# Performance work log

Hardware: AMD Instinct MI355X
Metric: run time of the kernel (lower is better)

The kernel has to match this reference:

```python
import jax, jax.numpy as jnp
import numpy as np

N = 50000       # nodes
E = 800000      # edges (avg degree 16)
D_IN = 96
D_OUT = 96
K = 3           # Chebyshev order
EPS = 1e-5      # BatchNorm eps


def setup_inputs() -> dict:
    key = jax.random.key(0)
    k1, k2, k3 = jax.random.split(key, 3)
    x = jax.random.normal(k1, (N, D_IN), dtype=jnp.float32)
    edge_index = jax.random.randint(k2, (2, E), 0, N)
    # ChebConv weights: one [D_IN, D_OUT] matrix per Chebyshev order + shared bias
    W = jax.random.normal(k3, (K, D_IN, D_OUT), dtype=jnp.float32) * (1.0 / np.sqrt(D_IN))
    bias = jnp.zeros((D_OUT,), dtype=jnp.float32)
    # BatchNorm1d affine params
    gamma = jnp.ones((D_OUT,), dtype=jnp.float32)
    beta = jnp.zeros((D_OUT,), dtype=jnp.float32)
    return {"x": x, "edge_index": edge_index, "W": W, "bias": bias,
            "gamma": gamma, "beta": beta}


def _cheb_edge_norm(edge_index, num_nodes):
    # PyG ChebConv.__norm__ with normalization='sym', lambda_max=2.0:
    # L_hat = 2L/lambda_max - I = -D^{-1/2} A D^{-1/2} (self loops removed, diag 0)
    row, col = edge_index[0], edge_index[1]
    w = jnp.where(row != col, 1.0, 0.0)  # remove self loops (weight 0 == removed)
    deg = jax.ops.segment_sum(w, row, num_segments=num_nodes)
    dis = jnp.where(deg > 0, jax.lax.rsqrt(jnp.maximum(deg, 1e-12)), 0.0)
    return -dis[row] * w * dis[col]  # [E]


def reference(x, edge_index, W, bias, gamma, beta):
    row, col = edge_index[0], edge_index[1]
    norm = _cheb_edge_norm(edge_index, N)

    def prop(h):  # sparse L_hat @ h via gather + scatter-add
        return jax.ops.segment_sum(norm[:, None] * h[row], col, num_segments=N)

    # Chebyshev recursion: T0 = x, T1 = L_hat x, Tk = 2 L_hat T_{k-1} - T_{k-2}
    Tx0 = x
    out = Tx0 @ W[0]
    Tx1 = prop(Tx0)
    out = out + Tx1 @ W[1]
    for k in range(2, K):
        Tx2 = 2.0 * prop(Tx1) - Tx0
        out = out + Tx2 @ W[k]
        Tx0, Tx1 = Tx1, Tx2
    out = out + bias

    # BatchNorm1d (training mode: batch stats over nodes, biased variance)
    mean = out.mean(axis=0)
    var = out.var(axis=0)
    return (out - mean) * jax.lax.rsqrt(var + EPS) * gamma + beta
```

## Files before the change

### kernel.cpp

```cpp
#include <hip/hip_runtime.h>

#define N_NODES 50000
#define N_EDGES 800000
#define D 96
#define DH 48
#define CAP 48
#define HG 64
#define W4 (N_NODES / 4)
#define EPS_BN 1e-5f

typedef short bf16x8 __attribute__((ext_vector_type(8)));
typedef float f32x4  __attribute__((ext_vector_type(4)));
union frag_cvt { uint4 u; bf16x8 f; };

__device__ __forceinline__ unsigned pack_bf16(float a, float b) {
    unsigned ua = __float_as_uint(a), ub = __float_as_uint(b);
    ua = (ua + 0x7fffu + ((ua >> 16) & 1u)) >> 16;
    ub = (ub + 0x7fffu + ((ub >> 16) & 1u)) >> 16;
    return (ua & 0xffffu) | (ub << 16);
}
__device__ __forceinline__ unsigned bf16_hi_bits(float a) {
    unsigned u = __float_as_uint(a);
    return (u + 0x7fffu + ((u >> 16) & 1u)) & 0xffff0000u;
}
__device__ __forceinline__ float bf16_lo(unsigned u) { return __uint_as_float(u << 16); }
__device__ __forceinline__ float bf16_hi(unsigned u) { return __uint_as_float(u & 0xffff0000u); }

#define CB ((N_NODES * DH + 1023) / 1024)
__global__ __launch_bounds__(1024) void prep_hist_kernel(
        const int* __restrict__ ei, unsigned* __restrict__ rowpart,
        unsigned* __restrict__ colpart, const float* __restrict__ x,
        unsigned* __restrict__ xh, const float* __restrict__ W,
        unsigned* __restrict__ wswz) {
    if (blockIdx.x < HG) {
        __shared__ unsigned h[W4];
        const int chunk = N_EDGES / HG;
        const int e0 = blockIdx.x * chunk;
        int rs[13], cs[13];
        int n = 0;
        for (int e = e0 + threadIdx.x; e < e0 + chunk; e += 1024, ++n) {
            rs[n] = ei[e];
            cs[n] = ei[N_EDGES + e];
        }
        for (int w = threadIdx.x; w < W4; w += 1024) h[w] = 0;
        __syncthreads();
        for (int i = 0; i < n; ++i)
            if (rs[i] != cs[i]) atomicAdd(&h[rs[i] >> 2], 1u << ((rs[i] & 3) * 8));
        __syncthreads();
        unsigned* rp = rowpart + (size_t)blockIdx.x * W4;
        for (int w = threadIdx.x; w < W4; w += 1024) rp[w] = h[w];
        __syncthreads();
        for (int w = threadIdx.x; w < W4; w += 1024) h[w] = 0;
        __syncthreads();
        for (int i = 0; i < n; ++i)
            if (rs[i] != cs[i]) atomicAdd(&h[cs[i] >> 2], 1u << ((cs[i] & 3) * 8));
        __syncthreads();
        unsigned* cp = colpart + (size_t)blockIdx.x * W4;
        for (int w = threadIdx.x; w < W4; w += 1024) cp[w] = h[w];
    } else if (blockIdx.x < HG + CB) {
        int t = (blockIdx.x - HG) * 1024 + threadIdx.x;
        if (t >= N_NODES * DH) return;
        float2 v = ((const float2*)x)[t];
        xh[t] = pack_bf16(v.x, v.y);
    } else {
        int t = (blockIdx.x - HG - CB) * 1024 + threadIdx.x;
        if (t >= 3 * 3 * 6 * 64) return;
        int lane = t & 63;
        int rest = t >> 6;
        int tile = rest % 6; rest /= 6;
        int q    = rest % 3;
        int s    = rest / 3;
        int n     = tile * 16 + (lane & 15);
        int kbase = q * 32 + (lane >> 4) * 8;
        uint4 u;
        const float* Wk = W + ((size_t)s * D + kbase) * D + n;
        u.x = pack_bf16(Wk[0 * D], Wk[1 * D]);
        u.y = pack_bf16(Wk[2 * D], Wk[3 * D]);
        u.z = pack_bf16(Wk[4 * D], Wk[5 * D]);
        u.w = pack_bf16(Wk[6 * D], Wk[7 * D]);
        ((uint4*)wswz)[t] = u;
    }
}

__global__ void reduce_kernel(unsigned* __restrict__ colpart,
                              const unsigned* __restrict__ rowpart,
                              int* __restrict__ cnt, float* __restrict__ dis,
                              float* __restrict__ stats) {
    if (blockIdx.x == 0 && threadIdx.x < 2 * D) stats[threadIdx.x] = 0.f;
    int w = blockIdx.x * blockDim.x + threadIdx.x;
    if (w >= W4) return;
    unsigned run = 0;
    for (int b = 0; b < HG; ++b) {
        unsigned v = colpart[(size_t)b * W4 + w];
        colpart[(size_t)b * W4 + w] = run;
        run += v;
    }
    int4 c4;
    c4.x = run & 0xffu; c4.y = (run >> 8) & 0xffu;
    c4.z = (run >> 16) & 0xffu; c4.w = run >> 24;
    ((int4*)cnt)[w] = c4;
    unsigned s0 = 0, s1 = 0, s2 = 0, s3 = 0;
    for (int b = 0; b < HG; ++b) {
        unsigned v = rowpart[(size_t)b * W4 + w];
        s0 += v & 0xffu; s1 += (v >> 8) & 0xffu;
        s2 += (v >> 16) & 0xffu; s3 += v >> 24;
    }
    float4 o;
    o.x = s0 ? rsqrtf((float)s0) : 0.f;
    o.y = s1 ? rsqrtf((float)s1) : 0.f;
    o.z = s2 ? rsqrtf((float)s2) : 0.f;
    o.w = s3 ? rsqrtf((float)s3) : 0.f;
    ((float4*)dis)[w] = o;
}

__global__ __launch_bounds__(1024) void place_kernel(const int* __restrict__ ei,
                                                     const unsigned* __restrict__ colpart,
                                                     const float* __restrict__ dis,
                                                     unsigned* __restrict__ ent) {
    __shared__ unsigned h[W4];
    const unsigned* pref = colpart + (size_t)blockIdx.x * W4;
    for (int w = threadIdx.x; w < W4; w += 1024) h[w] = pref[w];
    __syncthreads();
    const int chunk = N_EDGES / HG;
    const int e0 = blockIdx.x * chunk;
    for (int e = e0 + threadIdx.x; e < e0 + chunk; e += 1024) {
        int r = ei[e];
        int c = ei[N_EDGES + e];
        if (r == c) continue;
        float w = -dis[r] * dis[c];
        int sh = (c & 3) * 8;
        unsigned old = atomicAdd(&h[c >> 2], 1u << sh);
        int pos = (old >> sh) & 0xff;
        if (pos < CAP) ent[c * CAP + pos] = bf16_hi_bits(w) | (unsigned)r;
    }
}

template <int MODE>
__global__ __launch_bounds__(256) void prop_gather_kernel(
        const int* __restrict__ cnt_arr, const unsigned* __restrict__ ent,
        const unsigned* __restrict__ hp, const float* __restrict__ x,
        unsigned* __restrict__ out_h) {
    int nodeA = blockIdx.x * 8 + (threadIdx.x >> 6) * 2;
    int nodeB = nodeA + 1;
    int lane = threadIdx.x & 63;
    if (nodeA >= N_NODES) return;
    const int cl = (lane < DH) ? lane : (lane - DH);
    int cntA = cnt_arr[nodeA]; if (cntA > CAP) cntA = CAP;
    int cntB = cnt_arr[nodeB]; if (cntB > CAP) cntB = CAP;
    unsigned elA = (lane < cntA) ? ent[nodeA * CAP + lane] : 0u;
    unsigned elB = (lane < cntB) ? ent[nodeB * CAP + lane] : 0u;
    float a0 = 0.f, a1 = 0.f, b0 = 0.f, b1 = 0.f;
    int cmax = cntA > cntB ? cntA : cntB;
    for (int j = 0; j < cmax; j += 24) {
        unsigned eeA[24], eeB[24];
        #pragma unroll
        for (int i = 0; i < 24; ++i) {
            eeA[i] = (unsigned)__shfl((int)elA, j + i, 64);
            eeB[i] = (unsigned)__shfl((int)elB, j + i, 64);
        }
        unsigned uuA[24], uuB[24];
        #pragma unroll
        for (int i = 0; i < 24; ++i)
            uuA[i] = hp[(eeA[i] & 0xffffu) * DH + cl];
        #pragma unroll
        for (int i = 0; i < 24; ++i)
            uuB[i] = hp[(eeB[i] & 0xffffu) * DH + cl];
        #pragma unroll
        for (int i = 0; i < 24; ++i) {
            float wA = __uint_as_float(eeA[i] & 0xffff0000u);
            a0 = fmaf(wA, bf16_lo(uuA[i]), a0);
            a1 = fmaf(wA, bf16_hi(uuA[i]), a1);
            float wB = __uint_as_float(eeB[i] & 0xffff0000u);
            b0 = fmaf(wB, bf16_lo(uuB[i]), b0);
            b1 = fmaf(wB, bf16_hi(uuB[i]), b1);
        }
    }
    if (lane < DH) {
        if (MODE == 0) {
            out_h[nodeA * DH + cl] = pack_bf16(a0, a1);
            out_h[nodeB * DH + cl] = pack_bf16(b0, b1);
        } else {
            float2 xA = ((const float2*)x)[nodeA * DH + cl];
            float2 xB = ((const float2*)x)[nodeB * DH + cl];
            out_h[nodeA * DH + cl] = pack_bf16(fmaf(2.f, a0, -xA.x),
                                               fmaf(2.f, a1, -xA.y));
            out_h[nodeB * DH + cl] = pack_bf16(fmaf(2.f, b0, -xB.x),
                                               fmaf(2.f, b1, -xB.y));
        }
    }
}

__global__ __launch_bounds__(256) void mfma_gemm_kernel(
        const unsigned* __restrict__ xh, const unsigned* __restrict__ t1h,
        const unsigned* __restrict__ t2h, const unsigned* __restrict__ wswz,
        float* __restrict__ out, float* __restrict__ stats) {
    const int wave = threadIdx.x >> 6;
    const int lane = threadIdx.x & 63;
    const int m    = lane & 15;
    const int kg   = lane >> 4;
    const int nb   = blockIdx.x * 128 + wave * 32;
    __shared__ float ssum[4][D], ssq[4][D];

    int arow0 = nb + m;       if (arow0 > N_NODES - 1) arow0 = N_NODES - 1;
    int arow1 = nb + 16 + m;  if (arow1 > N_NODES - 1) arow1 = N_NODES - 1;

    const unsigned* bases[3] = {xh, t1h, t2h};

    f32x4 acc[2][6];
    #pragma unroll
    for (int h = 0; h < 2; ++h)
        #pragma unroll
        for (int t = 0; t < 6; ++t) acc[h][t] = (f32x4){0.f, 0.f, 0.f, 0.f};

    #pragma unroll
    for (int s = 0; s < 3; ++s) {
        const unsigned* A0 = bases[s] + (size_t)arow0 * DH + kg * 4;
        const unsigned* A1 = bases[s] + (size_t)arow1 * DH + kg * 4;
        #pragma unroll
        for (int q = 0; q < 3; ++q) {
            frag_cvt a0, a1;
            a0.u = *(const uint4*)(A0 + q * 16);
            a1.u = *(const uint4*)(A1 + q * 16);
            const uint4* Bp = (const uint4*)wswz + (size_t)((s * 3 + q) * 6) * 64 + lane;
            #pragma unroll
            for (int t = 0; t < 6; ++t) {
                frag_cvt b;
                b.u = Bp[t * 64];
                acc[0][t] = __builtin_amdgcn_mfma_f32_16x16x32_bf16(a0.f, b.f, acc[0][t], 0, 0, 0);
                acc[1][t] = __builtin_amdgcn_mfma_f32_16x16x32_bf16(a1.f, b.f, acc[1][t], 0, 0, 0);
            }
        }
    }

    #pragma unroll
    for (int t = 0; t < 6; ++t) {
        int col = t * 16 + m;
        float s1 = 0.f, s2 = 0.f;
        #pragma unroll
        for (int h = 0; h < 2; ++h) {
            #pragma unroll
            for (int r = 0; r < 4; ++r) {
                int g = nb + h * 16 + kg * 4 + r;
                if (g < N_NODES) {
                    float o = acc[h][t][r];
                    out[(size_t)g * D + col] = o;
                    s1 += o;
                    s2 += o * o;
                }
            }
        }
        s1 += __shfl_xor(s1, 16, 64); s2 += __shfl_xor(s2, 16, 64);
        s1 += __shfl_xor(s1, 32, 64); s2 += __shfl_xor(s2, 32, 64);
        if (lane < 16) { ssum[wave][col] = s1; ssq[wave][col] = s2; }
    }
    __syncthreads();
    if (threadIdx.x < D) {
        int c = threadIdx.x;
        float s1 = ssum[0][c] + ssum[1][c] + ssum[2][c] + ssum[3][c];
        float s2 = ssq [0][c] + ssq [1][c] + ssq [2][c] + ssq [3][c];
        atomicAdd(&stats[c],     s1);
        atomicAdd(&stats[D + c], s2);
    }
}

__global__ void bn_kernel(float* __restrict__ o, const float* __restrict__ stats,
                          const float* __restrict__ gamma, const float* __restrict__ beta) {
    __shared__ __align__(16) float s_sc[D], s_sh[D];
    if (threadIdx.x < D) {
        int c = threadIdx.x;
        const float invN = 1.f / (float)N_NODES;
        float mean = stats[c] * invN;
        float var  = stats[D + c] * invN - mean * mean;
        float inv  = rsqrtf(fmaxf(var, 0.f) + EPS_BN);
        float sc   = gamma[c] * inv;
        s_sc[c] = sc;
        s_sh[c] = beta[c] - mean * sc;
    }
    __syncthreads();
    int t = blockIdx.x * blockDim.x + threadIdx.x;
    if (t >= N_NODES * (D / 4)) return;
    int c4 = t % (D / 4);
    float4 v  = ((float4*)o)[t];
    float4 sc = *(const float4*)(s_sc + c4 * 4);
    float4 sh = *(const float4*)(s_sh + c4 * 4);
    v.x = fmaf(v.x, sc.x, sh.x);
    v.y = fmaf(v.y, sc.y, sh.y);
    v.z = fmaf(v.z, sc.z, sh.z);
    v.w = fmaf(v.w, sc.w, sh.w);
    ((float4*)o)[t] = v;
}

extern "C" void kernel_launch(void* const* d_in, const int* in_sizes, int n_in,
                              void* d_out, int out_size, void* d_ws, size_t ws_size,
                              hipStream_t stream) {
    const float* x     = (const float*)d_in[0];
    const int*   ei    = (const int*)  d_in[1];
    const float* W     = (const float*)d_in[2];
    const float* bias  = (const float*)d_in[3];
    const float* gamma = (const float*)d_in[4];
    const float* beta  = (const float*)d_in[5];
    float* out = (float*)d_out;
    (void)bias;

    float*    stats   = (float*)d_ws;
    float*    dis     = stats + 2 * D;
    int*      cnt     = (int*)(dis + N_NODES);
    unsigned* ent     = (unsigned*)(cnt + N_NODES);
    unsigned* xh      = ent + (size_t)N_NODES * CAP;
    unsigned* t1h     = xh  + (size_t)N_NODES * DH;
    unsigned* t2h     = t1h + (size_t)N_NODES * DH;
    unsigned* wswz    = t2h + (size_t)N_NODES * DH;
    unsigned* rowpart = t2h;
    unsigned* colpart = t2h + (size_t)HG * W4;

    prep_hist_kernel<<<HG + CB + 4, 1024, 0, stream>>>(ei, rowpart, colpart,
                                                       x, xh, W, wswz);
    reduce_kernel<<<(W4 + 255) / 256, 256, 0, stream>>>(colpart, rowpart, cnt,
                                                        dis, stats);
    place_kernel<<<HG, 1024, 0, stream>>>(ei, colpart, dis, ent);

    const int prop_blocks = N_NODES / 8;
    prop_gather_kernel<0><<<prop_blocks, 256, 0, stream>>>(cnt, ent, xh,  nullptr, t1h);
    prop_gather_kernel<1><<<prop_blocks, 256, 0, stream>>>(cnt, ent, t1h, x,       t2h);

    mfma_gemm_kernel<<<(N_NODES + 127) / 128, 256, 0, stream>>>(
        xh, t1h, t2h, wswz, out, stats);

    bn_kernel<<<(N_NODES * (D / 4) + 255) / 256, 256, 0, stream>>>(out, stats, gamma, beta);
}
```

Measured before the change: 214.9 us.

## Replace LDS partitioned histogram CSR build with global atomics

Replaces the three-kernel graph preprocessing (per-block LDS byte-packed histograms, prefix reduction, LDS-based placement) with a memset, one prep kernel doing global atomic degree counts alongside the casts, and a placement kernel using global atomicAdd on per-column slot counters. This removes the serial 64-way prefix loop and the partial-histogram traffic, and saves a launch. The cost is contended global atomics over 800k edges instead of cheap LDS atomics. Edge order within each node's bucket also becomes nondeterministic, which changes the floating-point summation order.

```diff
diff --git a/kernel.cpp b/kernel.cpp
--- a/kernel.cpp
+++ b/kernel.cpp
@@ -5,8 +5,6 @@
 #define D 96
 #define DH 48
 #define CAP 48
-#define HG 64
-#define W4 (N_NODES / 4)
 #define EPS_BN 1e-5f
 
 typedef short bf16x8 __attribute__((ext_vector_type(8)));
@@ -26,44 +24,23 @@
 __device__ __forceinline__ float bf16_lo(unsigned u) { return __uint_as_float(u << 16); }
 __device__ __forceinline__ float bf16_hi(unsigned u) { return __uint_as_float(u & 0xffff0000u); }
 
-#define CB ((N_NODES * DH + 1023) / 1024)
-__global__ __launch_bounds__(1024) void prep_hist_kernel(
-        const int* __restrict__ ei, unsigned* __restrict__ rowpart,
-        unsigned* __restrict__ colpart, const float* __restrict__ x,
-        unsigned* __restrict__ xh, const float* __restrict__ W,
-        unsigned* __restrict__ wswz) {
-    if (blockIdx.x < HG) {
-        __shared__ unsigned h[W4];
-        const int chunk = N_EDGES / HG;
-        const int e0 = blockIdx.x * chunk;
-        int rs[13], cs[13];
-        int n = 0;
-        for (int e = e0 + threadIdx.x; e < e0 + chunk; e += 1024, ++n) {
-            rs[n] = ei[e];
-            cs[n] = ei[N_EDGES + e];
-        }
-        for (int w = threadIdx.x; w < W4; w += 1024) h[w] = 0;
-        __syncthreads();
-        for (int i = 0; i < n; ++i)
-            if (rs[i] != cs[i]) atomicAdd(&h[rs[i] >> 2], 1u << ((rs[i] & 3) * 8));
-        __syncthreads();
-        unsigned* rp = rowpart + (size_t)blockIdx.x * W4;
-        for (int w = threadIdx.x; w < W4; w += 1024) rp[w] = h[w];
-        __syncthreads();
-        for (int w = threadIdx.x; w < W4; w += 1024) h[w] = 0;
-        __syncthreads();
-        for (int i = 0; i < n; ++i)
-            if (rs[i] != cs[i]) atomicAdd(&h[cs[i] >> 2], 1u << ((cs[i] & 3) * 8));
-        __syncthreads();
-        unsigned* cp = colpart + (size_t)blockIdx.x * W4;
-        for (int w = threadIdx.x; w < W4; w += 1024) cp[w] = h[w];
-    } else if (blockIdx.x < HG + CB) {
-        int t = (blockIdx.x - HG) * 1024 + threadIdx.x;
-        if (t >= N_NODES * DH) return;
+#define CAST_BLK (N_NODES * DH / 256)
+#define EDGE_BLK (N_EDGES / 256)
+__global__ __launch_bounds__(256) void prep2_kernel(
+        const int* __restrict__ ei, int* __restrict__ deg,
+        const float* __restrict__ x, unsigned* __restrict__ xh,
+        const float* __restrict__ W, unsigned* __restrict__ wswz) {
+    if (blockIdx.x < CAST_BLK) {
+        int t = blockIdx.x * 256 + threadIdx.x;
         float2 v = ((const float2*)x)[t];
         xh[t] = pack_bf16(v.x, v.y);
+    } else if (blockIdx.x < CAST_BLK + EDGE_BLK) {
+        int e = (blockIdx.x - CAST_BLK) * 256 + threadIdx.x;
+        int r = ei[e];
+        int c = ei[N_EDGES + e];
+        if (r != c) atomicAdd(&deg[r], 1);
     } else {
-        int t = (blockIdx.x - HG - CB) * 1024 + threadIdx.x;
+        int t = (blockIdx.x - CAST_BLK - EDGE_BLK) * 256 + threadIdx.x;
         if (t >= 3 * 3 * 6 * 64) return;
         int lane = t & 63;
         int rest = t >> 6;
@@ -82,57 +59,18 @@
     }
 }
 
-__global__ void reduce_kernel(unsigned* __restrict__ colpart,
-                              const unsigned* __restrict__ rowpart,
-                              int* __restrict__ cnt, float* __restrict__ dis,
-                              float* __restrict__ stats) {
-    if (blockIdx.x == 0 && threadIdx.x < 2 * D) stats[threadIdx.x] = 0.f;
-    int w = blockIdx.x * blockDim.x + threadIdx.x;
-    if (w >= W4) return;
-    unsigned run = 0;
-    for (int b = 0; b < HG; ++b) {
-        unsigned v = colpart[(size_t)b * W4 + w];
-        colpart[(size_t)b * W4 + w] = run;
-        run += v;
-    }
-    int4 c4;
-    c4.x = run & 0xffu; c4.y = (run >> 8) & 0xffu;
-    c4.z = (run >> 16) & 0xffu; c4.w = run >> 24;
-    ((int4*)cnt)[w] = c4;
-    unsigned s0 = 0, s1 = 0, s2 = 0, s3 = 0;
-    for (int b = 0; b < HG; ++b) {
-        unsigned v = rowpart[(size_t)b * W4 + w];
-        s0 += v & 0xffu; s1 += (v >> 8) & 0xffu;
-        s2 += (v >> 16) & 0xffu; s3 += v >> 24;
-    }
-    float4 o;
-    o.x = s0 ? rsqrtf((float)s0) : 0.f;
-    o.y = s1 ? rsqrtf((float)s1) : 0.f;
-    o.z = s2 ? rsqrtf((float)s2) : 0.f;
-    o.w = s3 ? rsqrtf((float)s3) : 0.f;
-    ((float4*)dis)[w] = o;
-}
-
-__global__ __launch_bounds__(1024) void place_kernel(const int* __restrict__ ei,
-                                                     const unsigned* __restrict__ colpart,
-                                                     const float* __restrict__ dis,
-                                                     unsigned* __restrict__ ent) {
-    __shared__ unsigned h[W4];
-    const unsigned* pref = colpart + (size_t)blockIdx.x * W4;
-    for (int w = threadIdx.x; w < W4; w += 1024) h[w] = pref[w];
-    __syncthreads();
-    const int chunk = N_EDGES / HG;
-    const int e0 = blockIdx.x * chunk;
-    for (int e = e0 + threadIdx.x; e < e0 + chunk; e += 1024) {
-        int r = ei[e];
-        int c = ei[N_EDGES + e];
-        if (r == c) continue;
-        float w = -dis[r] * dis[c];
-        int sh = (c & 3) * 8;
-        unsigned old = atomicAdd(&h[c >> 2], 1u << sh);
-        int pos = (old >> sh) & 0xff;
-        if (pos < CAP) ent[c * CAP + pos] = bf16_hi_bits(w) | (unsigned)r;
-    }
+__global__ __launch_bounds__(256) void place2_kernel(
+        const int* __restrict__ ei, const int* __restrict__ deg,
+        int* __restrict__ pos, unsigned* __restrict__ ent) {
+    int e = blockIdx.x * 256 + threadIdx.x;
+    int r = ei[e];
+    int c = ei[N_EDGES + e];
+    if (r == c) return;
+    int dr = deg[r];
+    int dc = deg[c];
+    float w = (dc > 0) ? -rsqrtf((float)dr) * rsqrtf((float)dc) : 0.f;
+    int p = atomicAdd(&pos[c], 1);
+    if (p < CAP) ent[c * CAP + p] = bf16_hi_bits(w) | (unsigned)r;
 }
 
 template <int MODE>
@@ -302,26 +240,25 @@
     float* out = (float*)d_out;
     (void)bias;
 
-    float*    stats   = (float*)d_ws;
-    float*    dis     = stats + 2 * D;
-    int*      cnt     = (int*)(dis + N_NODES);
-    unsigned* ent     = (unsigned*)(cnt + N_NODES);
-    unsigned* xh      = ent + (size_t)N_NODES * CAP;
-    unsigned* t1h     = xh  + (size_t)N_NODES * DH;
-    unsigned* t2h     = t1h + (size_t)N_NODES * DH;
-    unsigned* wswz    = t2h + (size_t)N_NODES * DH;
-    unsigned* rowpart = t2h;
-    unsigned* colpart = t2h + (size_t)HG * W4;
-
-    prep_hist_kernel<<<HG + CB + 4, 1024, 0, stream>>>(ei, rowpart, colpart,
-                                                       x, xh, W, wswz);
-    reduce_kernel<<<(W4 + 255) / 256, 256, 0, stream>>>(colpart, rowpart, cnt,
-                                                        dis, stats);
-    place_kernel<<<HG, 1024, 0, stream>>>(ei, colpart, dis, ent);
+    float*    stats = (float*)d_ws;
+    int*      deg   = (int*)(stats + 2 * D);
+    int*      pos   = deg + N_NODES;
+    unsigned* ent   = (unsigned*)(pos + N_NODES);
+    unsigned* xh    = ent + (size_t)N_NODES * CAP;
+    unsigned* t1h   = xh  + (size_t)N_NODES * DH;
+    unsigned* t2h   = t1h + (size_t)N_NODES * DH;
+    unsigned* wswz  = t2h + (size_t)N_NODES * DH;
+
+    hipMemsetAsync(stats, 0, (2 * D + 2 * N_NODES) * sizeof(int), stream);
+
+    prep2_kernel<<<CAST_BLK + EDGE_BLK + 14, 256, 0, stream>>>(
+        ei, deg, x, xh, W, wswz);
+
+    place2_kernel<<<EDGE_BLK, 256, 0, stream>>>(ei, deg, pos, ent);
 
     const int prop_blocks = N_NODES / 8;
-    prop_gather_kernel<0><<<prop_blocks, 256, 0, stream>>>(cnt, ent, xh,  nullptr, t1h);
-    prop_gather_kernel<1><<<prop_blocks, 256, 0, stream>>>(cnt, ent, t1h, x,       t2h);
+    prop_gather_kernel<0><<<prop_blocks, 256, 0, stream>>>(pos, ent, xh,  nullptr, t1h);
+    prop_gather_kernel<1><<<prop_blocks, 256, 0, stream>>>(pos, ent, t1h, x,       t2h);
 
     mfma_gemm_kernel<<<(N_NODES + 127) / 128, 256, 0, stream>>>(
         xh, t1h, t2h, wswz, out, stats);
```

New measurement: 239.3 us. 11.4% more time.

## Fuse GEMM with BatchNorm via grid barrier and split row/col histograms

Applied to the files above, without the earlier changes.

The GEMM kernel now keeps its accumulators in registers, adds per-column sums to global stats, waits at a software grid-wide barrier, then applies the BatchNorm scale and shift and writes the output once. This removes the separate BN kernel along with its read and re-write of the full output. The histogram stage is also split so separate blocks build the row and column histograms in parallel instead of one block doing both in sequence. The risk is that the software barrier (391 blocks of 256 threads) deadlocks if not all blocks are resident at once, and spinning blocks waste time.

```diff
diff --git a/kernel.cpp b/kernel.cpp
--- a/kernel.cpp
+++ b/kernel.cpp
@@ -26,44 +26,71 @@
 __device__ __forceinline__ float bf16_lo(unsigned u) { return __uint_as_float(u << 16); }
 __device__ __forceinline__ float bf16_hi(unsigned u) { return __uint_as_float(u & 0xffff0000u); }
 
+__device__ unsigned g_cnt;
+__device__ unsigned g_gen;
+
+__device__ __forceinline__ void grid_barrier(unsigned nblk) {
+    __syncthreads();
+    if (threadIdx.x == 0) {
+        __threadfence();
+        unsigned g = __hip_atomic_load(&g_gen, __ATOMIC_RELAXED,
+                                       __HIP_MEMORY_SCOPE_AGENT);
+        unsigned arrived = __hip_atomic_fetch_add(&g_cnt, 1u,
+                                                  __ATOMIC_ACQ_REL,
+                                                  __HIP_MEMORY_SCOPE_AGENT);
+        if (arrived == nblk - 1u) {
+            __hip_atomic_store(&g_cnt, 0u, __ATOMIC_RELAXED,
+                               __HIP_MEMORY_SCOPE_AGENT);
+            __hip_atomic_store(&g_gen, g + 1u, __ATOMIC_RELEASE,
+                               __HIP_MEMORY_SCOPE_AGENT);
+        } else {
+            while (__hip_atomic_load(&g_gen, __ATOMIC_ACQUIRE,
+                                     __HIP_MEMORY_SCOPE_AGENT) == g)
+                __builtin_amdgcn_s_sleep(2);
+        }
+        __threadfence();
+    }
+    __syncthreads();
+}
+
 #define CB ((N_NODES * DH + 1023) / 1024)
+#define HB 128
 __global__ __launch_bounds__(1024) void prep_hist_kernel(
         const int* __restrict__ ei, unsigned* __restrict__ rowpart,
         unsigned* __restrict__ colpart, const float* __restrict__ x,
         unsigned* __restrict__ xh, const float* __restrict__ W,
         unsigned* __restrict__ wswz) {
-    if (blockIdx.x < HG) {
+    if (blockIdx.x < HB) {
         __shared__ unsigned h[W4];
+        const int cb = blockIdx.x & 63;
+        const bool isRow = blockIdx.x < 64;
         const int chunk = N_EDGES / HG;
-        const int e0 = blockIdx.x * chunk;
+        const int e0 = cb * chunk;
         int rs[13], cs[13];
         int n = 0;
-        for (int e = e0 + threadIdx.x; e < e0 + chunk; e += 1024, ++n) {
+        for (int e = e0 + (int)threadIdx.x; e < e0 + chunk; e += 1024, ++n) {
             rs[n] = ei[e];
             cs[n] = ei[N_EDGES + e];
         }
         for (int w = threadIdx.x; w < W4; w += 1024) h[w] = 0;
         __syncthreads();
-        for (int i = 0; i < n; ++i)
-            if (rs[i] != cs[i]) atomicAdd(&h[rs[i] >> 2], 1u << ((rs[i] & 3) * 8));
+        if (isRow) {
+            for (int i = 0; i < n; ++i)
+                if (rs[i] != cs[i]) atomicAdd(&h[rs[i] >> 2], 1u << ((rs[i] & 3) * 8));
+        } else {
+            for (int i = 0; i < n; ++i)
+                if (rs[i] != cs[i]) atomicAdd(&h[cs[i] >> 2], 1u << ((cs[i] & 3) * 8));
+        }
         __syncthreads();
-        unsigned* rp = rowpart + (size_t)blockIdx.x * W4;
-        for (int w = threadIdx.x; w < W4; w += 1024) rp[w] = h[w];
-        __syncthreads();
-        for (int w = threadIdx.x; w < W4; w += 1024) h[w] = 0;
-        __syncthreads();
-        for (int i = 0; i < n; ++i)
-            if (rs[i] != cs[i]) atomicAdd(&h[cs[i] >> 2], 1u << ((cs[i] & 3) * 8));
-        __syncthreads();
-        unsigned* cp = colpart + (size_t)blockIdx.x * W4;
-        for (int w = threadIdx.x; w < W4; w += 1024) cp[w] = h[w];
-    } else if (blockIdx.x < HG + CB) {
-        int t = (blockIdx.x - HG) * 1024 + threadIdx.x;
+        unsigned* dst = (isRow ? rowpart : colpart) + (size_t)cb * W4;
+        for (int w = threadIdx.x; w < W4; w += 1024) dst[w] = h[w];
+    } else if (blockIdx.x < HB + CB) {
+        int t = (blockIdx.x - HB) * 1024 + threadIdx.x;
         if (t >= N_NODES * DH) return;
         float2 v = ((const float2*)x)[t];
         xh[t] = pack_bf16(v.x, v.y);
     } else {
-        int t = (blockIdx.x - HG - CB) * 1024 + threadIdx.x;
+        int t = (blockIdx.x - HB - CB) * 1024 + threadIdx.x;
         if (t >= 3 * 3 * 6 * 64) return;
         int lane = t & 63;
         int rest = t >> 6;
@@ -190,10 +217,11 @@
     }
 }
 
-__global__ __launch_bounds__(256) void mfma_gemm_kernel(
+__global__ __launch_bounds__(256) void gemm_bn_kernel(
         const unsigned* __restrict__ xh, const unsigned* __restrict__ t1h,
         const unsigned* __restrict__ t2h, const unsigned* __restrict__ wswz,
-        float* __restrict__ out, float* __restrict__ stats) {
+        float* __restrict__ out, float* __restrict__ stats,
+        const float* __restrict__ gamma, const float* __restrict__ beta) {
     const int wave = threadIdx.x >> 6;
     const int lane = threadIdx.x & 63;
     const int m    = lane & 15;
@@ -243,7 +271,6 @@
                 int g = nb + h * 16 + kg * 4 + r;
                 if (g < N_NODES) {
                     float o = acc[h][t][r];
-                    out[(size_t)g * D + col] = o;
                     s1 += o;
                     s2 += o * o;
                 }
@@ -256,38 +283,31 @@
     __syncthreads();
     if (threadIdx.x < D) {
         int c = threadIdx.x;
-        float s1 = ssum[0][c] + ssum[1][c] + ssum[2][c] + ssum[3][c];
-        float s2 = ssq [0][c] + ssq [1][c] + ssq [2][c] + ssq [3][c];
-        atomicAdd(&stats[c],     s1);
-        atomicAdd(&stats[D + c], s2);
-    }
-}
-
-__global__ void bn_kernel(float* __restrict__ o, const float* __restrict__ stats,
-                          const float* __restrict__ gamma, const float* __restrict__ beta) {
-    __shared__ __align__(16) float s_sc[D], s_sh[D];
-    if (threadIdx.x < D) {
-        int c = threadIdx.x;
-        const float invN = 1.f / (float)N_NODES;
-        float mean = stats[c] * invN;
-        float var  = stats[D + c] * invN - mean * mean;
+        atomicAdd(&stats[c],     ssum[0][c] + ssum[1][c] + ssum[2][c] + ssum[3][c]);
+        atomicAdd(&stats[D + c], ssq [0][c] + ssq [1][c] + ssq [2][c] + ssq [3][c]);
+    }
+
+    grid_barrier(gridDim.x);
+
+    const float invN = 1.f / (float)N_NODES;
+    #pragma unroll
+    for (int t = 0; t < 6; ++t) {
+        int col = t * 16 + m;
+        float mean = stats[col] * invN;
+        float var  = stats[D + col] * invN - mean * mean;
         float inv  = rsqrtf(fmaxf(var, 0.f) + EPS_BN);
-        float sc   = gamma[c] * inv;
-        s_sc[c] = sc;
-        s_sh[c] = beta[c] - mean * sc;
-    }
-    __syncthreads();
-    int t = blockIdx.x * blockDim.x + threadIdx.x;
-    if (t >= N_NODES * (D / 4)) return;
-    int c4 = t % (D / 4);
-    float4 v  = ((float4*)o)[t];
-    float4 sc = *(const float4*)(s_sc + c4 * 4);
-    float4 sh = *(const float4*)(s_sh + c4 * 4);
-    v.x = fmaf(v.x, sc.x, sh.x);
-    v.y = fmaf(v.y, sc.y, sh.y);
-    v.z = fmaf(v.z, sc.z, sh.z);
-    v.w = fmaf(v.w, sc.w, sh.w);
-    ((float4*)o)[t] = v;
+        float sc   = gamma[col] * inv;
+        float sh   = beta[col] - mean * sc;
+        #pragma unroll
+        for (int h = 0; h < 2; ++h) {
+            #pragma unroll
+            for (int r = 0; r < 4; ++r) {
+                int g = nb + h * 16 + kg * 4 + r;
+                if (g < N_NODES)
+                    out[(size_t)g * D + col] = fmaf(acc[h][t][r], sc, sh);
+            }
+        }
+    }
 }
 
 extern "C" void kernel_launch(void* const* d_in, const int* in_sizes, int n_in,
@@ -313,7 +333,7 @@
     unsigned* rowpart = t2h;
     unsigned* colpart = t2h + (size_t)HG * W4;
 
-    prep_hist_kernel<<<HG + CB + 4, 1024, 0, stream>>>(ei, rowpart, colpart,
+    prep_hist_kernel<<<HB + CB + 4, 1024, 0, stream>>>(ei, rowpart, colpart,
                                                        x, xh, W, wswz);
     reduce_kernel<<<(W4 + 255) / 256, 256, 0, stream>>>(colpart, rowpart, cnt,
                                                         dis, stats);
@@ -323,8 +343,6 @@
     prop_gather_kernel<0><<<prop_blocks, 256, 0, stream>>>(cnt, ent, xh,  nullptr, t1h);
     prop_gather_kernel<1><<<prop_blocks, 256, 0, stream>>>(cnt, ent, t1h, x,       t2h);
 
-    mfma_gemm_kernel<<<(N_NODES + 127) / 128, 256, 0, stream>>>(
-        xh, t1h, t2h, wswz, out, stats);
-
-    bn_kernel<<<(N_NODES * (D / 4) + 255) / 256, 256, 0, stream>>>(out, stats, gamma, beta);
-}
+    gemm_bn_kernel<<<(N_NODES + 127) / 128, 256, 0, stream>>>(
+        xh, t1h, t2h, wswz, out, stats, gamma, beta);
+}
```

After: 251.1 us. 16.8% more time.
